# Performance work log

Hardware: AMD Instinct MI355X
Metric: run time of the kernel (lower is better)

The kernel has to match this reference:

```python
import jax, jax.numpy as jnp
import numpy as np

NUM_GROUPS = 32
EPS = 1e-5
HEAD_DIM = 64

def group_norm(x, w, b):
    # x: [B,C,H,W]; normalize within 32 groups over (C//32, H, W)
    B, C, H, W = x.shape
    xg = x.reshape(B, NUM_GROUPS, C // NUM_GROUPS, H, W)
    mu = xg.mean(axis=(2, 3, 4), keepdims=True)
    var = xg.var(axis=(2, 3, 4), keepdims=True)
    xn = ((xg - mu) / jnp.sqrt(var + EPS)).reshape(B, C, H, W)
    return xn * w[None, :, None, None] + b[None, :, None, None]

def conv1x1(x, w, b):
    # w: [Cout, Cin], b: [Cout]
    return jnp.einsum('bchw,oc->bohw', x, w) + b[None, :, None, None]

def setup_inputs() -> dict:
    key = jax.random.key(0)
    ks = jax.random.split(key, 12)
    B, C, Cc, H, W = 16, 512, 512, 32, 32
    s = 0.02
    return {
        'x': jax.random.normal(ks[0], (B, C, H, W), jnp.float32),
        'context': jax.random.normal(ks[1], (B, Cc, H, W), jnp.float32),
        'norm_q_w': jnp.ones((C,), jnp.float32),
        'norm_q_b': jnp.zeros((C,), jnp.float32),
        'norm_kv_w': jnp.ones((Cc,), jnp.float32),
        'norm_kv_b': jnp.zeros((Cc,), jnp.float32),
        'conv_q_w': jax.random.normal(ks[2], (C, C), jnp.float32) * s,
        'conv_q_b': jnp.zeros((C,), jnp.float32),
        'conv_kv_w': jax.random.normal(ks[3], (2 * C, Cc), jnp.float32) * s,
        'conv_kv_b': jnp.zeros((2 * C,), jnp.float32),
        'proj_w': jax.random.normal(ks[4], (C, C), jnp.float32) * s,
        'proj_b': jnp.zeros((C,), jnp.float32),
    }

def reference(x, context, norm_q_w, norm_q_b, norm_kv_w, norm_kv_b,
              conv_q_w, conv_q_b, conv_kv_w, conv_kv_b, proj_w, proj_b):
    B, C, H, W = x.shape
    nh = max(1, C // HEAD_DIM)
    hd = C // nh
    q = conv1x1(group_norm(x, norm_q_w, norm_q_b), conv_q_w, conv_q_b)
    kv = conv1x1(group_norm(context, norm_kv_w, norm_kv_b), conv_kv_w, conv_kv_b)
    k, v = jnp.split(kv, 2, axis=1)
    L = H * W
    q = q.reshape(B, nh, hd, L)
    k = k.reshape(B, nh, hd, L)
    v = v.reshape(B, nh, hd, L)
    attn = jnp.einsum('bhdi,bhdj->bhij', q, k) * (hd ** -0.5)
    attn = jax.nn.softmax(attn, axis=-1)
    out = jnp.einsum('bhij,bhdj->bhdi', attn, v)
    return x + conv1x1(out.reshape(B, C, H, W), proj_w, proj_b)
```

## Files before the change

### kernel.cpp

```cpp
#include <hip/hip_runtime.h>
#include <hip/hip_bf16.h>

typedef short v8s __attribute__((ext_vector_type(8)));
typedef float v4f __attribute__((ext_vector_type(4)));
typedef float v16f __attribute__((ext_vector_type(16)));
typedef __hip_bfloat16 bf16;

__device__ __forceinline__ float b2f(bf16 h) { return __bfloat162float(h); }
__device__ __forceinline__ bf16 f2b(float f) { return __float2bfloat16(f); }

#define QSCALE 0.18033688f

__device__ __forceinline__ void gll16(const void* g, void* l) {
    __builtin_amdgcn_global_load_lds(
        (const __attribute__((address_space(1))) void*)g,
        (__attribute__((address_space(3))) void*)l, 16, 0, 0);
}

__device__ __forceinline__ unsigned cvtpk(float lo, float hi_) {
    unsigned r;
    asm("v_cvt_pk_bf16_f32 %0, %1, %2" : "=v"(r) : "v"(lo), "v"(hi_));
    return r;
}

__device__ __forceinline__ void pl32swap(unsigned& a, unsigned& b) {
    asm("v_permlane32_swap_b32 %0, %1" : "+v"(a), "+v"(b));
}

__global__ __launch_bounds__(256) void gn_t_kernel(
    const float* __restrict__ x, const float* __restrict__ ctx,
    const float* __restrict__ qw, const float* __restrict__ qb,
    const float* __restrict__ kw, const float* __restrict__ kb,
    bf16* __restrict__ xnT, bf16* __restrict__ cnT)
{
    const int b = blockIdx.y, g = blockIdx.x, z = blockIdx.z, c0 = g * 16;
    const float* src = z ? ctx : x;
    const float* gw  = z ? kw : qw;
    const float* gb  = z ? kb : qb;
    bf16* dst = z ? cnT : xnT;
    __shared__ __attribute__((aligned(16))) bf16 lx[16][1032];
    __shared__ float rS[4], rQ[4];
    __shared__ float sSc[16], sSh[16];
    const int t = threadIdx.x, wave = t >> 6, lane = t & 63;
    const float* xb = src + ((long)b * 512 + c0) * 1024;
    float sum = 0.f, sq = 0.f;
#pragma unroll
    for (int i = 0; i < 16; i++) {
        int q = t + i * 256;
        int ci = q >> 8, l0 = (q & 255) * 4;
        float4 v = *(const float4*)(xb + (long)ci * 1024 + l0);
        sum += v.x + v.y + v.z + v.w;
        sq  += v.x * v.x + v.y * v.y + v.z * v.z + v.w * v.w;
        union { short4 s4v; bf16 h[4]; } w;
        w.h[0] = f2b(v.x); w.h[1] = f2b(v.y); w.h[2] = f2b(v.z); w.h[3] = f2b(v.w);
        *(short4*)&lx[ci][l0] = w.s4v;
    }
#pragma unroll
    for (int off = 32; off > 0; off >>= 1) {
        sum += __shfl_down(sum, off);
        sq  += __shfl_down(sq, off);
    }
    if (lane == 0) { rS[wave] = sum; rQ[wave] = sq; }
    __syncthreads();
    if (t < 16) {
        float S = rS[0] + rS[1] + rS[2] + rS[3];
        float Q = rQ[0] + rQ[1] + rQ[2] + rQ[3];
        const float inv_n = 1.f / 16384.f;
        float mean = S * inv_n;
        float var  = Q * inv_n - mean * mean;
        float rstd = rsqrtf(var + 1e-5f);
        float w = gw[c0 + t];
        sSc[t] = rstd * w;
        sSh[t] = gb[c0 + t] - mean * rstd * w;
    }
    __syncthreads();
    {
        const int hf = t & 1, lg = t >> 1;
        const int ch0 = hf * 8, l0 = lg * 8;
        v8s rd[8];
#pragma unroll
        for (int r = 0; r < 8; r++)
            rd[r] = *(const v8s*)&lx[ch0 + r][l0];
        float sc[8], sh[8];
#pragma unroll
        for (int r = 0; r < 8; r++) { sc[r] = sSc[ch0 + r]; sh[r] = sSh[ch0 + r]; }
#pragma unroll
        for (int j = 0; j < 8; j++) {
            union { float4 f4; bf16 h[8]; } o_;
#pragma unroll
            for (int r = 0; r < 8; r++) {
                union { short s; bf16 h; } cv; cv.s = rd[r][j];
                o_.h[r] = f2b(b2f(cv.h) * sc[r] + sh[r]);
            }
            *(float4*)(dst + ((long)b * 1024 + l0 + j) * 512 + c0 + ch0) = o_.f4;
        }
    }
}

__global__ __launch_bounds__(256) void wconv_kernel(
    const float* __restrict__ a, const float* __restrict__ bsrc,
    const float* __restrict__ csrc, bf16* __restrict__ oa,
    bf16* __restrict__ ob, bf16* __restrict__ oc)
{
    int id = blockIdx.x * 256 + threadIdx.x;
    const float* src; bf16* dst; int off;
    if (id < 65536)       { src = a;    dst = oa; off = id; }
    else if (id < 196608) { src = bsrc; dst = ob; off = id - 65536; }
    else                  { src = csrc; dst = oc; off = id - 196608; }
    float4 v = ((const float4*)src)[off];
    union { short4 s4v; bf16 h[4]; } w;
    w.h[0] = f2b(v.x); w.h[1] = f2b(v.y); w.h[2] = f2b(v.z); w.h[3] = f2b(v.w);
    ((short4*)dst)[off] = w.s4v;
}

__global__ __launch_bounds__(256) void qkv_gemm_kernel(
    const bf16* __restrict__ xnT, const bf16* __restrict__ cnT,
    const bf16* __restrict__ wQ, const bf16* __restrict__ wKV,
    bf16* __restrict__ QT, bf16* __restrict__ KT, bf16* __restrict__ Vo,
    const float* __restrict__ cqb, const float* __restrict__ ckvb)
{
    const long PB = 512L * 1024;
    const int blk = blockIdx.x;
    const int xcd = blk & 7, idx = blk >> 3;
    const int half = idx / 96, rr = idx % 96;
    const int op = rr >> 5, bx = rr & 31;
    const int bz = xcd + 8 * half;
    const bf16* A; const bf16* B; bf16* C; const float* bias;
    int nBlkN, N, biasPerM; float scale;
    if (op == 0) {
        A = xnT + bz * PB; B = wQ;  C = QT + bz * PB; bias = cqb;
        nBlkN = 4; N = 512; biasPerM = 0; scale = QSCALE;
    } else if (op == 1) {
        A = cnT + bz * PB; B = wKV; C = KT + bz * PB; bias = ckvb;
        nBlkN = 4; N = 512; biasPerM = 0; scale = 1.0f;
    } else {
        A = wKV + 512L * 512; B = cnT + bz * PB; C = Vo + bz * PB; bias = ckvb + 512;
        nBlkN = 8; N = 1024; biasPerM = 1; scale = 1.0f;
    }
    const int m0 = (bx / nBlkN) * 128, n0 = (bx % nBlkN) * 128;
    __shared__ __attribute__((aligned(16))) bf16 lA[2][128][64];
    __shared__ __attribute__((aligned(16))) bf16 lB[2][128][64];
    const int t = threadIdx.x, wave = t >> 6, lane = t & 63;
    const int quad = lane >> 4, c = lane & 15;
    const int wm = (wave >> 1) * 64, wn = (wave & 1) * 64;
    const int rIS = lane >> 3;
    const int chG = (lane & 7) ^ rIS;
    const bf16* Ag[4]; const bf16* Bg[4]; int segr[4];
#pragma unroll
    for (int j = 0; j < 4; j++) {
        int seg = wave + j * 4;
        segr[j] = seg * 8;
        Ag[j] = A + (long)(m0 + segr[j] + rIS) * 512 + chG * 8;
        Bg[j] = B + (long)(n0 + segr[j] + rIS) * 512 + chG * 8;
    }
    auto issue = [&](int k0, int bi) {
#pragma unroll
        for (int j = 0; j < 4; j++) {
            gll16(Ag[j] + k0, &lA[bi][segr[j]][0]);
            gll16(Bg[j] + k0, &lB[bi][segr[j]][0]);
        }
    };
    v4f acc[4][4] = {};
    issue(0, 0);
    for (int kc = 0; kc < 8; kc++) {
        const int cur = kc & 1;
        asm volatile("s_waitcnt vmcnt(0)" ::: "memory");
        __builtin_amdgcn_s_barrier();
        __builtin_amdgcn_sched_barrier(0);
        if (kc < 7) issue((kc + 1) * 64, cur ^ 1);
#pragma unroll
        for (int kk = 0; kk < 2; kk++) {
            v8s af[4], bfr[4];
#pragma unroll
            for (int mt = 0; mt < 4; mt++)
                af[mt] = *(const v8s*)&lA[cur][wm + mt * 16 + c][((kk * 4 + quad) ^ (c & 7)) * 8];
#pragma unroll
            for (int nt = 0; nt < 4; nt++)
                bfr[nt] = *(const v8s*)&lB[cur][wn + nt * 16 + c][((kk * 4 + quad) ^ (c & 7)) * 8];
#pragma unroll
            for (int mt = 0; mt < 4; mt++)
#pragma unroll
                for (int nt = 0; nt < 4; nt++)
                    acc[mt][nt] = __builtin_amdgcn_mfma_f32_16x16x32_bf16(
                        af[mt], bfr[nt], acc[mt][nt], 0, 0, 0);
        }
    }
#pragma unroll
    for (int mt = 0; mt < 4; mt++) {
#pragma unroll
        for (int nt = 0; nt < 4; nt++) {
#pragma unroll
            for (int r = 0; r < 4; r++) {
                int row = m0 + wm + mt * 16 + quad * 4 + r;
                int col = n0 + wn + nt * 16 + c;
                float v = (acc[mt][nt][r] + (biasPerM ? bias[row] : bias[col])) * scale;
                C[(long)row * N + col] = f2b(v);
            }
        }
    }
}

__global__ __launch_bounds__(256) void gemm_proj_kernel(
    const bf16* __restrict__ A,
    const bf16* __restrict__ B, long sBb,
    float* __restrict__ C,
    const float* __restrict__ bias,
    const float* __restrict__ resid,
    int M, int N)
{
    const int blk = blockIdx.x;
    const int xcd = blk & 7, idx = blk >> 3;
    const int bz = xcd + 8 * (idx & 1);
    const int tile = idx >> 1;
    const int m0 = (tile >> 3) * 128, n0 = (tile & 7) * 128;
    const bf16* Bb = B + (long)bz * sBb;
    __shared__ __attribute__((aligned(16))) bf16 lA[2][128][64];
    __shared__ __attribute__((aligned(16))) bf16 lB[2][128][64];
    const int t = threadIdx.x, wave = t >> 6, lane = t & 63;
    const int quad = lane >> 4, c = lane & 15;
    const int wm = (wave >> 1) * 64, wn = (wave & 1) * 64;
    const int rIS = lane >> 3, chG = (lane & 7) ^ rIS;
    const bf16* Ag[4]; const bf16* Bg[4]; int segr[4];
#pragma unroll
    for (int j = 0; j < 4; j++) {
        int seg = wave + j * 4;
        segr[j] = seg * 8;
        Ag[j] = A + (long)(m0 + segr[j] + rIS) * 512 + chG * 8;
        Bg[j] = Bb + (long)(n0 + segr[j] + rIS) * 512 + chG * 8;
    }
    auto issue = [&](int k0, int bi) {
#pragma unroll
        for (int j = 0; j < 4; j++) {
            gll16(Ag[j] + k0, &lA[bi][segr[j]][0]);
            gll16(Bg[j] + k0, &lB[bi][segr[j]][0]);
        }
    };
    v4f acc[4][4] = {};
    issue(0, 0);
    for (int kc = 0; kc < 8; kc++) {
        const int cur = kc & 1;
        asm volatile("s_waitcnt vmcnt(0)" ::: "memory");
        __builtin_amdgcn_s_barrier();
        __builtin_amdgcn_sched_barrier(0);
        if (kc < 7) issue((kc + 1) * 64, cur ^ 1);
#pragma unroll
        for (int kk = 0; kk < 2; kk++) {
            v8s af[4], bfr[4];
#pragma unroll
            for (int mt = 0; mt < 4; mt++)
                af[mt] = *(const v8s*)&lA[cur][wm + mt * 16 + c][((kk * 4 + quad) ^ (c & 7)) * 8];
#pragma unroll
            for (int nt = 0; nt < 4; nt++)
                bfr[nt] = *(const v8s*)&lB[cur][wn + nt * 16 + c][((kk * 4 + quad) ^ (c & 7)) * 8];
#pragma unroll
            for (int mt = 0; mt < 4; mt++)
#pragma unroll
                for (int nt = 0; nt < 4; nt++)
                    acc[mt][nt] = __builtin_amdgcn_mfma_f32_16x16x32_bf16(
                        af[mt], bfr[nt], acc[mt][nt], 0, 0, 0);
        }
    }
#pragma unroll
    for (int mt = 0; mt < 4; mt++) {
#pragma unroll
        for (int nt = 0; nt < 4; nt++) {
#pragma unroll
            for (int r = 0; r < 4; r++) {
                int row = m0 + wm + mt * 16 + quad * 4 + r;
                int col = n0 + wn + nt * 16 + c;
                float v = acc[mt][nt][r] + bias[row]
                        + resid[(long)bz * ((long)M * N) + (long)row * N + col];
                C[(long)bz * ((long)M * N) + (long)row * N + col] = v;
            }
        }
    }
}

__global__ __launch_bounds__(256, 2) void attn_kernel(
    const bf16* QT, const bf16* __restrict__ KT,
    const bf16* __restrict__ V, bf16* AOT)
{
    const int nblk = blockIdx.x;
    const int s = nblk >> 3;
    const int it = s & 3;
    const int g = ((s >> 2) << 3) | (nblk & 7);
    const int h = g & 7, b = g >> 3;
    const int i0 = it * 256;
    __shared__ __attribute__((aligned(16))) bf16 lk[3][64][64];
    __shared__ __attribute__((aligned(16))) bf16 lv[3][64][64];
    const int t = threadIdx.x, wave = t >> 6, lane = t & 63;
    const int m31 = lane & 31, hi = lane >> 5;
    const int rIS = lane >> 3, chG = (lane & 7) ^ rIS;
    v8s qf[2][4];
#pragma unroll
    for (int iq = 0; iq < 2; iq++) {
        const bf16* Qb = QT + ((long)b * 1024 + i0 + wave * 64 + iq * 32 + m31) * 512 + h * 64;
#pragma unroll
        for (int ks = 0; ks < 4; ks++)
            qf[iq][ks] = *(const v8s*)(Qb + ks * 16 + hi * 8);
    }
    const bf16* Kg[2]; const bf16* Vg[2];
#pragma unroll
    for (int j = 0; j < 2; j++) {
        int seg = wave * 2 + j;
        Kg[j] = KT + ((long)b * 1024 + seg * 8 + rIS) * 512 + h * 64 + chG * 8;
        Vg[j] = V + ((long)b * 512 + h * 64 + seg * 8 + rIS) * 1024 + chG * 8;
    }
    auto issue = [&](int jtx, int bi) {
#pragma unroll
        for (int j = 0; j < 2; j++) {
            int seg = wave * 2 + j;
            gll16(Kg[j] + (long)jtx * 64 * 512, &lk[bi][seg * 8][0]);
            gll16(Vg[j] + (long)jtx * 64,      &lv[bi][seg * 8][0]);
        }
    };
    issue(0, 0);
    issue(1, 1);
    float lsum0 = 0.f, lsum1 = 0.f;
    v16f o00 = {}, o01 = {}, o10 = {}, o11 = {};

#define SMPV(sj0, sj1, JB)                                                     \
    {                                                                          \
        unsigned u0[8], u1[8];                                                 \
        _Pragma("unroll")                                                      \
        for (int k2 = 0; k2 < 8; k2++) {                                       \
            float p0l = __builtin_amdgcn_exp2f(sj0[2 * k2]);                   \
            float p0h = __builtin_amdgcn_exp2f(sj0[2 * k2 + 1]);               \
            float p1l = __builtin_amdgcn_exp2f(sj1[2 * k2]);                   \
            float p1h = __builtin_amdgcn_exp2f(sj1[2 * k2 + 1]);               \
            lsum0 += p0l + p0h; lsum1 += p1l + p1h;                            \
            u0[k2] = cvtpk(p0l, p0h); u1[k2] = cvtpk(p1l, p1h);                \
        }                                                                      \
        pl32swap(u0[0], u0[2]); pl32swap(u0[1], u0[3]);                        \
        pl32swap(u0[4], u0[6]); pl32swap(u0[5], u0[7]);                        \
        pl32swap(u1[0], u1[2]); pl32swap(u1[1], u1[3]);                        \
        pl32swap(u1[4], u1[6]); pl32swap(u1[5], u1[7]);                        \
        __builtin_amdgcn_s_setprio(1);                                         \
        _Pragma("unroll")                                                      \
        for (int kk = 0; kk < 2; kk++) {                                       \
            union { unsigned w[4]; v8s v; } pf0, pf1;                          \
            pf0.w[0] = u0[4 * kk + 0]; pf0.w[1] = u0[4 * kk + 1];              \
            pf0.w[2] = u0[4 * kk + 2]; pf0.w[3] = u0[4 * kk + 3];              \
            pf1.w[0] = u1[4 * kk + 0]; pf1.w[1] = u1[4 * kk + 1];              \
            pf1.w[2] = u1[4 * kk + 2]; pf1.w[3] = u1[4 * kk + 3];              \
            const int cc2 = ((JB) * 2 + kk) * 2 + hi;                          \
            v8s vf0 = *(const v8s*)&lv[cur][m31][(cc2 ^ (m31 & 7)) * 8];       \
            o00 = __builtin_amdgcn_mfma_f32_32x32x16_bf16(vf0, pf0.v, o00, 0, 0, 0); \
            o10 = __builtin_amdgcn_mfma_f32_32x32x16_bf16(vf0, pf1.v, o10, 0, 0, 0); \
            v8s vf1 = *(const v8s*)&lv[cur][32 + m31][(cc2 ^ (m31 & 7)) * 8];  \
            o01 = __builtin_amdgcn_mfma_f32_32x32x16_bf16(vf1, pf0.v, o01, 0, 0, 0); \
            o11 = __builtin_amdgcn_mfma_f32_32x32x16_bf16(vf1, pf1.v, o11, 0, 0, 0); \
        }                                                                      \
        __builtin_amdgcn_s_setprio(0);                                         \
    }

    for (int jt = 0; jt < 16; jt++) {
        const int cur = jt % 3;
        asm volatile("s_waitcnt vmcnt(4)" ::: "memory");
        __builtin_amdgcn_s_barrier();
        __builtin_amdgcn_sched_barrier(0);
        issue((jt + 2) & 15, (jt + 2) % 3);
        v16f s00 = {}, s01 = {}, s10 = {}, s11 = {};
        __builtin_amdgcn_s_setprio(1);
#pragma unroll
        for (int ks = 0; ks < 4; ks++) {
            const int chs = ((ks * 2 + hi) ^ (m31 & 7)) * 8;
            v8s kf0 = *(const v8s*)&lk[cur][m31][chs];
            v8s kf1 = *(const v8s*)&lk[cur][32 + m31][chs];
            s00 = __builtin_amdgcn_mfma_f32_32x32x16_bf16(kf0, qf[0][ks], s00, 0, 0, 0);
            s01 = __builtin_amdgcn_mfma_f32_32x32x16_bf16(kf0, qf[1][ks], s01, 0, 0, 0);
            s10 = __builtin_amdgcn_mfma_f32_32x32x16_bf16(kf1, qf[0][ks], s10, 0, 0, 0);
            s11 = __builtin_amdgcn_mfma_f32_32x32x16_bf16(kf1, qf[1][ks], s11, 0, 0, 0);
        }
        __builtin_amdgcn_s_setprio(0);
        SMPV(s00, s01, 0)
        SMPV(s10, s11, 1)
    }
#undef SMPV
    {
        float lt0 = lsum0 + __shfl_xor(lsum0, 32);
        float lt1 = lsum1 + __shfl_xor(lsum1, 32);
        float inv0 = 1.f / lt0, inv1 = 1.f / lt1;
#pragma unroll
        for (int iq = 0; iq < 2; iq++) {
            float inv = iq ? inv1 : inv0;
            const v16f& oa = iq ? o10 : o00;
            const v16f& ob = iq ? o11 : o01;
            bf16* Ob = AOT + ((long)b * 1024 + i0 + wave * 64 + iq * 32 + m31) * 512 + h * 64;
#pragma unroll
            for (int gq = 0; gq < 4; gq++) {
                union { short4 s4v; bf16 hh[4]; } w0, w1;
#pragma unroll
                for (int k = 0; k < 4; k++) {
                    w0.hh[k] = f2b(oa[gq * 4 + k] * inv);
                    w1.hh[k] = f2b(ob[gq * 4 + k] * inv);
                }
                *(short4*)(Ob + gq * 8 + hi * 4)      = w0.s4v;
                *(short4*)(Ob + 32 + gq * 8 + hi * 4) = w1.s4v;
            }
        }
    }
}

extern "C" void kernel_launch(void* const* d_in, const int* in_sizes, int n_in,
                              void* d_out, int out_size, void* d_ws, size_t ws_size,
                              hipStream_t stream)
{
    const float* x    = (const float*)d_in[0];
    const float* ctx  = (const float*)d_in[1];
    const float* nqw  = (const float*)d_in[2];
    const float* nqb  = (const float*)d_in[3];
    const float* nkw  = (const float*)d_in[4];
    const float* nkb  = (const float*)d_in[5];
    const float* cqw  = (const float*)d_in[6];
    const float* cqb  = (const float*)d_in[7];
    const float* ckvw = (const float*)d_in[8];
    const float* ckvb = (const float*)d_in[9];
    const float* pw   = (const float*)d_in[10];
    const float* pb   = (const float*)d_in[11];
    float* out = (float*)d_out;
    bf16* ws  = (bf16*)d_ws;

    const long PB  = 512L * 1024;
    const long TOT = 16L * PB;
    bf16* s0 = ws;
    bf16* s1 = ws + TOT;
    bf16* s2 = ws + 2 * TOT;
    bf16* s3 = ws + 3 * TOT;
    bf16* s4 = ws + 4 * TOT;
    bf16* wQ  = ws + 5 * TOT;
    bf16* wKV = wQ + 262144;
    bf16* wP  = wKV + 524288;

    dim3 blk(256);
    gn_t_kernel<<<dim3(32, 16, 2), blk, 0, stream>>>(
        x, ctx, nqw, nqb, nkw, nkb, s0, s1);
    wconv_kernel<<<dim3(1024), blk, 0, stream>>>(cqw, ckvw, pw, wQ, wKV, wP);
    qkv_gemm_kernel<<<dim3(1536), blk, 0, stream>>>(
        s0, s1, wQ, wKV, s2, s3, s4, cqb, ckvb);
    attn_kernel<<<dim3(512), blk, 0, stream>>>(s2, s3, s4, s2);
    gemm_proj_kernel<<<dim3(512), blk, 0, stream>>>(
        wP, s2, PB, out, pb, x, 512, 1024);
}
```

Measured before the change: 234.3 us.

## Halve attention query tile per block to double grid and occupancy

The attention kernel now gives each wave 32 query rows instead of 64, so a block covers 128 queries and the grid grows from 512 to 1024 blocks, with launch bounds raised to 4 blocks per CU. The V buffer is cut to double buffering with its own prefetch schedule, while K stays triple-buffered, which lowers LDS use enough to fit more blocks. Register pressure per thread drops because there are half as many accumulators. In exchange, each K/V tile loaded into LDS is reused by fewer queries, so total K/V traffic from global memory doubles, and the shallower V prefetch may expose more load latency.

```diff
diff --git a/kernel.cpp b/kernel.cpp
--- a/kernel.cpp
+++ b/kernel.cpp
@@ -276,29 +276,26 @@
     }
 }
 
-__global__ __launch_bounds__(256, 2) void attn_kernel(
+__global__ __launch_bounds__(256, 4) void attn_kernel(
     const bf16* QT, const bf16* __restrict__ KT,
     const bf16* __restrict__ V, bf16* AOT)
 {
     const int nblk = blockIdx.x;
     const int s = nblk >> 3;
-    const int it = s & 3;
-    const int g = ((s >> 2) << 3) | (nblk & 7);
+    const int it = s & 7;
+    const int g = ((s >> 3) << 3) | (nblk & 7);
     const int h = g & 7, b = g >> 3;
-    const int i0 = it * 256;
+    const int i0 = it * 128;
     __shared__ __attribute__((aligned(16))) bf16 lk[3][64][64];
-    __shared__ __attribute__((aligned(16))) bf16 lv[3][64][64];
+    __shared__ __attribute__((aligned(16))) bf16 lv[2][64][64];
     const int t = threadIdx.x, wave = t >> 6, lane = t & 63;
     const int m31 = lane & 31, hi = lane >> 5;
     const int rIS = lane >> 3, chG = (lane & 7) ^ rIS;
-    v8s qf[2][4];
-#pragma unroll
-    for (int iq = 0; iq < 2; iq++) {
-        const bf16* Qb = QT + ((long)b * 1024 + i0 + wave * 64 + iq * 32 + m31) * 512 + h * 64;
-#pragma unroll
-        for (int ks = 0; ks < 4; ks++)
-            qf[iq][ks] = *(const v8s*)(Qb + ks * 16 + hi * 8);
-    }
+    const bf16* Qb = QT + ((long)b * 1024 + i0 + wave * 32 + m31) * 512 + h * 64;
+    v8s qf[4];
+#pragma unroll
+    for (int ks = 0; ks < 4; ks++)
+        qf[ks] = *(const v8s*)(Qb + ks * 16 + hi * 8);
     const bf16* Kg[2]; const bf16* Vg[2];
 #pragma unroll
     for (int j = 0; j < 2; j++) {
@@ -306,98 +303,85 @@
         Kg[j] = KT + ((long)b * 1024 + seg * 8 + rIS) * 512 + h * 64 + chG * 8;
         Vg[j] = V + ((long)b * 512 + h * 64 + seg * 8 + rIS) * 1024 + chG * 8;
     }
-    auto issue = [&](int jtx, int bi) {
-#pragma unroll
-        for (int j = 0; j < 2; j++) {
-            int seg = wave * 2 + j;
-            gll16(Kg[j] + (long)jtx * 64 * 512, &lk[bi][seg * 8][0]);
-            gll16(Vg[j] + (long)jtx * 64,      &lv[bi][seg * 8][0]);
-        }
+    auto issueK = [&](int jtx, int bi) {
+#pragma unroll
+        for (int j = 0; j < 2; j++)
+            gll16(Kg[j] + (long)jtx * 64 * 512, &lk[bi][(wave * 2 + j) * 8][0]);
     };
-    issue(0, 0);
-    issue(1, 1);
-    float lsum0 = 0.f, lsum1 = 0.f;
-    v16f o00 = {}, o01 = {}, o10 = {}, o11 = {};
-
-#define SMPV(sj0, sj1, JB)                                                     \
+    auto issueV = [&](int jtx, int bi) {
+#pragma unroll
+        for (int j = 0; j < 2; j++)
+            gll16(Vg[j] + (long)jtx * 64, &lv[bi][(wave * 2 + j) * 8][0]);
+    };
+    issueV(0, 0);
+    issueK(0, 0);
+    issueK(1, 1);
+    float lsum = 0.f;
+    v16f o0 = {}, o1 = {};
+
+#define SMPV(sj, JB)                                                           \
     {                                                                          \
-        unsigned u0[8], u1[8];                                                 \
+        unsigned u[8];                                                         \
         _Pragma("unroll")                                                      \
         for (int k2 = 0; k2 < 8; k2++) {                                       \
-            float p0l = __builtin_amdgcn_exp2f(sj0[2 * k2]);                   \
-            float p0h = __builtin_amdgcn_exp2f(sj0[2 * k2 + 1]);               \
-            float p1l = __builtin_amdgcn_exp2f(sj1[2 * k2]);                   \
-            float p1h = __builtin_amdgcn_exp2f(sj1[2 * k2 + 1]);               \
-            lsum0 += p0l + p0h; lsum1 += p1l + p1h;                            \
-            u0[k2] = cvtpk(p0l, p0h); u1[k2] = cvtpk(p1l, p1h);                \
+            float pl = __builtin_amdgcn_exp2f(sj[2 * k2]);                     \
+            float ph = __builtin_amdgcn_exp2f(sj[2 * k2 + 1]);                 \
+            lsum += pl + ph;                                                   \
+            u[k2] = cvtpk(pl, ph);                                             \
         }                                                                      \
-        pl32swap(u0[0], u0[2]); pl32swap(u0[1], u0[3]);                        \
-        pl32swap(u0[4], u0[6]); pl32swap(u0[5], u0[7]);                        \
-        pl32swap(u1[0], u1[2]); pl32swap(u1[1], u1[3]);                        \
-        pl32swap(u1[4], u1[6]); pl32swap(u1[5], u1[7]);                        \
+        pl32swap(u[0], u[2]); pl32swap(u[1], u[3]);                            \
+        pl32swap(u[4], u[6]); pl32swap(u[5], u[7]);                            \
         __builtin_amdgcn_s_setprio(1);                                         \
         _Pragma("unroll")                                                      \
         for (int kk = 0; kk < 2; kk++) {                                       \
-            union { unsigned w[4]; v8s v; } pf0, pf1;                          \
-            pf0.w[0] = u0[4 * kk + 0]; pf0.w[1] = u0[4 * kk + 1];              \
-            pf0.w[2] = u0[4 * kk + 2]; pf0.w[3] = u0[4 * kk + 3];              \
-            pf1.w[0] = u1[4 * kk + 0]; pf1.w[1] = u1[4 * kk + 1];              \
-            pf1.w[2] = u1[4 * kk + 2]; pf1.w[3] = u1[4 * kk + 3];              \
+            union { unsigned w[4]; v8s v; } pf;                                \
+            pf.w[0] = u[4 * kk + 0]; pf.w[1] = u[4 * kk + 1];                  \
+            pf.w[2] = u[4 * kk + 2]; pf.w[3] = u[4 * kk + 3];                  \
             const int cc2 = ((JB) * 2 + kk) * 2 + hi;                          \
-            v8s vf0 = *(const v8s*)&lv[cur][m31][(cc2 ^ (m31 & 7)) * 8];       \
-            o00 = __builtin_amdgcn_mfma_f32_32x32x16_bf16(vf0, pf0.v, o00, 0, 0, 0); \
-            o10 = __builtin_amdgcn_mfma_f32_32x32x16_bf16(vf0, pf1.v, o10, 0, 0, 0); \
-            v8s vf1 = *(const v8s*)&lv[cur][32 + m31][(cc2 ^ (m31 & 7)) * 8];  \
-            o01 = __builtin_amdgcn_mfma_f32_32x32x16_bf16(vf1, pf0.v, o01, 0, 0, 0); \
-            o11 = __builtin_amdgcn_mfma_f32_32x32x16_bf16(vf1, pf1.v, o11, 0, 0, 0); \
+            v8s vf0 = *(const v8s*)&lv[vcur][m31][(cc2 ^ (m31 & 7)) * 8];      \
+            o0 = __builtin_amdgcn_mfma_f32_32x32x16_bf16(vf0, pf.v, o0, 0, 0, 0); \
+            v8s vf1 = *(const v8s*)&lv[vcur][32 + m31][(cc2 ^ (m31 & 7)) * 8]; \
+            o1 = __builtin_amdgcn_mfma_f32_32x32x16_bf16(vf1, pf.v, o1, 0, 0, 0); \
         }                                                                      \
         __builtin_amdgcn_s_setprio(0);                                         \
     }
 
     for (int jt = 0; jt < 16; jt++) {
-        const int cur = jt % 3;
-        asm volatile("s_waitcnt vmcnt(4)" ::: "memory");
+        const int kcur = jt % 3, vcur = jt & 1;
+        asm volatile("s_waitcnt vmcnt(2)" ::: "memory");
         __builtin_amdgcn_s_barrier();
         __builtin_amdgcn_sched_barrier(0);
-        issue((jt + 2) & 15, (jt + 2) % 3);
-        v16f s00 = {}, s01 = {}, s10 = {}, s11 = {};
+        issueV((jt + 1) & 15, vcur ^ 1);
+        issueK((jt + 2) & 15, (jt + 2) % 3);
+        v16f s0 = {}, s1 = {};
         __builtin_amdgcn_s_setprio(1);
 #pragma unroll
         for (int ks = 0; ks < 4; ks++) {
             const int chs = ((ks * 2 + hi) ^ (m31 & 7)) * 8;
-            v8s kf0 = *(const v8s*)&lk[cur][m31][chs];
-            v8s kf1 = *(const v8s*)&lk[cur][32 + m31][chs];
-            s00 = __builtin_amdgcn_mfma_f32_32x32x16_bf16(kf0, qf[0][ks], s00, 0, 0, 0);
-            s01 = __builtin_amdgcn_mfma_f32_32x32x16_bf16(kf0, qf[1][ks], s01, 0, 0, 0);
-            s10 = __builtin_amdgcn_mfma_f32_32x32x16_bf16(kf1, qf[0][ks], s10, 0, 0, 0);
-            s11 = __builtin_amdgcn_mfma_f32_32x32x16_bf16(kf1, qf[1][ks], s11, 0, 0, 0);
+            v8s kf0 = *(const v8s*)&lk[kcur][m31][chs];
+            v8s kf1 = *(const v8s*)&lk[kcur][32 + m31][chs];
+            s0 = __builtin_amdgcn_mfma_f32_32x32x16_bf16(kf0, qf[ks], s0, 0, 0, 0);
+            s1 = __builtin_amdgcn_mfma_f32_32x32x16_bf16(kf1, qf[ks], s1, 0, 0, 0);
         }
         __builtin_amdgcn_s_setprio(0);
-        SMPV(s00, s01, 0)
-        SMPV(s10, s11, 1)
+        SMPV(s0, 0)
+        SMPV(s1, 1)
     }
 #undef SMPV
     {
-        float lt0 = lsum0 + __shfl_xor(lsum0, 32);
-        float lt1 = lsum1 + __shfl_xor(lsum1, 32);
-        float inv0 = 1.f / lt0, inv1 = 1.f / lt1;
-#pragma unroll
-        for (int iq = 0; iq < 2; iq++) {
-            float inv = iq ? inv1 : inv0;
-            const v16f& oa = iq ? o10 : o00;
-            const v16f& ob = iq ? o11 : o01;
-            bf16* Ob = AOT + ((long)b * 1024 + i0 + wave * 64 + iq * 32 + m31) * 512 + h * 64;
-#pragma unroll
-            for (int gq = 0; gq < 4; gq++) {
-                union { short4 s4v; bf16 hh[4]; } w0, w1;
-#pragma unroll
-                for (int k = 0; k < 4; k++) {
-                    w0.hh[k] = f2b(oa[gq * 4 + k] * inv);
-                    w1.hh[k] = f2b(ob[gq * 4 + k] * inv);
-                }
-                *(short4*)(Ob + gq * 8 + hi * 4)      = w0.s4v;
-                *(short4*)(Ob + 32 + gq * 8 + hi * 4) = w1.s4v;
+        float lt = lsum + __shfl_xor(lsum, 32);
+        float inv = 1.f / lt;
+        bf16* Ob = AOT + ((long)b * 1024 + i0 + wave * 32 + m31) * 512 + h * 64;
+#pragma unroll
+        for (int gq = 0; gq < 4; gq++) {
+            union { short4 s4v; bf16 hh[4]; } w0, w1;
+#pragma unroll
+            for (int k = 0; k < 4; k++) {
+                w0.hh[k] = f2b(o0[gq * 4 + k] * inv);
+                w1.hh[k] = f2b(o1[gq * 4 + k] * inv);
             }
+            *(short4*)(Ob + gq * 8 + hi * 4)      = w0.s4v;
+            *(short4*)(Ob + 32 + gq * 8 + hi * 4) = w1.s4v;
         }
     }
 }
@@ -438,7 +422,7 @@
     wconv_kernel<<<dim3(1024), blk, 0, stream>>>(cqw, ckvw, pw, wQ, wKV, wP);
     qkv_gemm_kernel<<<dim3(1536), blk, 0, stream>>>(
         s0, s1, wQ, wKV, s2, s3, s4, cqb, ckvb);
-    attn_kernel<<<dim3(512), blk, 0, stream>>>(s2, s3, s4, s2);
+    attn_kernel<<<dim3(1024), blk, 0, stream>>>(s2, s3, s4, s2);
     gemm_proj_kernel<<<dim3(512), blk, 0, stream>>>(
         wP, s2, PB, out, pb, x, 512, 1024);
 }
```

After: 245.9 us. 1.05x slower.

## Triple-buffer QKV GEMM with 32-wide K tiles; drop setprio in attention

Applied to the files above, without the earlier changes.

The QKV projection GEMM moves from a double-buffered 64-wide K tile with a full vmcnt(0) wait to a triple-buffered 32-wide K tile. Two loads stay in flight, with a partial vmcnt wait and a new XOR swizzle matching the narrower rows. This should hide global-to-LDS latency better and cut LDS use, at the cost of twice as many barriers per K loop. Separately, the s_setprio raises around the MFMA sections in the attention kernel are removed. The tail iterations wrap around and issue redundant loads into unused buffers.

```diff
diff --git a/kernel.cpp b/kernel.cpp
--- a/kernel.cpp
+++ b/kernel.cpp
@@ -138,52 +138,51 @@
         nBlkN = 8; N = 1024; biasPerM = 1; scale = 1.0f;
     }
     const int m0 = (bx / nBlkN) * 128, n0 = (bx % nBlkN) * 128;
-    __shared__ __attribute__((aligned(16))) bf16 lA[2][128][64];
-    __shared__ __attribute__((aligned(16))) bf16 lB[2][128][64];
+    __shared__ __attribute__((aligned(16))) bf16 lA[3][128][32];
+    __shared__ __attribute__((aligned(16))) bf16 lB[3][128][32];
     const int t = threadIdx.x, wave = t >> 6, lane = t & 63;
     const int quad = lane >> 4, c = lane & 15;
     const int wm = (wave >> 1) * 64, wn = (wave & 1) * 64;
-    const int rIS = lane >> 3;
-    const int chG = (lane & 7) ^ rIS;
-    const bf16* Ag[4]; const bf16* Bg[4]; int segr[4];
-#pragma unroll
-    for (int j = 0; j < 4; j++) {
-        int seg = wave + j * 4;
-        segr[j] = seg * 8;
-        Ag[j] = A + (long)(m0 + segr[j] + rIS) * 512 + chG * 8;
-        Bg[j] = B + (long)(n0 + segr[j] + rIS) * 512 + chG * 8;
+    const int r16 = lane >> 2;
+    const int c4 = lane & 3;
+    const int cswz = c4 ^ (r16 & 3) ^ ((r16 >> 2) & 1);
+    const bf16* Ag[2]; const bf16* Bg[2];
+#pragma unroll
+    for (int j = 0; j < 2; j++) {
+        int seg = wave * 2 + j;
+        Ag[j] = A + (long)(m0 + seg * 16 + r16) * 512 + cswz * 8;
+        Bg[j] = B + (long)(n0 + seg * 16 + r16) * 512 + cswz * 8;
     }
     auto issue = [&](int k0, int bi) {
 #pragma unroll
-        for (int j = 0; j < 4; j++) {
-            gll16(Ag[j] + k0, &lA[bi][segr[j]][0]);
-            gll16(Bg[j] + k0, &lB[bi][segr[j]][0]);
+        for (int j = 0; j < 2; j++) {
+            gll16(Ag[j] + k0, &lA[bi][(wave * 2 + j) * 16][0]);
+            gll16(Bg[j] + k0, &lB[bi][(wave * 2 + j) * 16][0]);
         }
     };
     v4f acc[4][4] = {};
     issue(0, 0);
-    for (int kc = 0; kc < 8; kc++) {
-        const int cur = kc & 1;
-        asm volatile("s_waitcnt vmcnt(0)" ::: "memory");
+    issue(32, 1);
+    const int rdsw = (quad ^ (c & 3) ^ ((c >> 2) & 1)) * 8;
+    for (int kc = 0; kc < 16; kc++) {
+        const int cur = kc % 3;
+        asm volatile("s_waitcnt vmcnt(4)" ::: "memory");
         __builtin_amdgcn_s_barrier();
         __builtin_amdgcn_sched_barrier(0);
-        if (kc < 7) issue((kc + 1) * 64, cur ^ 1);
-#pragma unroll
-        for (int kk = 0; kk < 2; kk++) {
-            v8s af[4], bfr[4];
-#pragma unroll
-            for (int mt = 0; mt < 4; mt++)
-                af[mt] = *(const v8s*)&lA[cur][wm + mt * 16 + c][((kk * 4 + quad) ^ (c & 7)) * 8];
+        issue(((kc + 2) & 15) * 32, (kc + 2) % 3);
+        v8s af[4], bfr[4];
+#pragma unroll
+        for (int mt = 0; mt < 4; mt++)
+            af[mt] = *(const v8s*)&lA[cur][wm + mt * 16 + c][rdsw];
+#pragma unroll
+        for (int nt = 0; nt < 4; nt++)
+            bfr[nt] = *(const v8s*)&lB[cur][wn + nt * 16 + c][rdsw];
+#pragma unroll
+        for (int mt = 0; mt < 4; mt++)
 #pragma unroll
             for (int nt = 0; nt < 4; nt++)
-                bfr[nt] = *(const v8s*)&lB[cur][wn + nt * 16 + c][((kk * 4 + quad) ^ (c & 7)) * 8];
-#pragma unroll
-            for (int mt = 0; mt < 4; mt++)
-#pragma unroll
-                for (int nt = 0; nt < 4; nt++)
-                    acc[mt][nt] = __builtin_amdgcn_mfma_f32_16x16x32_bf16(
-                        af[mt], bfr[nt], acc[mt][nt], 0, 0, 0);
-        }
+                acc[mt][nt] = __builtin_amdgcn_mfma_f32_16x16x32_bf16(
+                    af[mt], bfr[nt], acc[mt][nt], 0, 0, 0);
     }
 #pragma unroll
     for (int mt = 0; mt < 4; mt++) {
@@ -335,7 +334,6 @@
         pl32swap(u0[4], u0[6]); pl32swap(u0[5], u0[7]);                        \
         pl32swap(u1[0], u1[2]); pl32swap(u1[1], u1[3]);                        \
         pl32swap(u1[4], u1[6]); pl32swap(u1[5], u1[7]);                        \
-        __builtin_amdgcn_s_setprio(1);                                         \
         _Pragma("unroll")                                                      \
         for (int kk = 0; kk < 2; kk++) {                                       \
             union { unsigned w[4]; v8s v; } pf0, pf1;                          \
@@ -351,7 +349,6 @@
             o01 = __builtin_amdgcn_mfma_f32_32x32x16_bf16(vf1, pf0.v, o01, 0, 0, 0); \
             o11 = __builtin_amdgcn_mfma_f32_32x32x16_bf16(vf1, pf1.v, o11, 0, 0, 0); \
         }                                                                      \
-        __builtin_amdgcn_s_setprio(0);                                         \
     }
 
     for (int jt = 0; jt < 16; jt++) {
@@ -361,7 +358,6 @@
         __builtin_amdgcn_sched_barrier(0);
         issue((jt + 2) & 15, (jt + 2) % 3);
         v16f s00 = {}, s01 = {}, s10 = {}, s11 = {};
-        __builtin_amdgcn_s_setprio(1);
 #pragma unroll
         for (int ks = 0; ks < 4; ks++) {
             const int chs = ((ks * 2 + hi) ^ (m31 & 7)) * 8;
@@ -372,7 +368,6 @@
             s10 = __builtin_amdgcn_mfma_f32_32x32x16_bf16(kf1, qf[0][ks], s10, 0, 0, 0);
             s11 = __builtin_amdgcn_mfma_f32_32x32x16_bf16(kf1, qf[1][ks], s11, 0, 0, 0);
         }
-        __builtin_amdgcn_s_setprio(0);
         SMPV(s00, s01, 0)
         SMPV(s10, s11, 1)
     }
```

Result: no change. 237.1 us (+1.2%).
